# Optimization experiments

Hardware: AMD Instinct MI355X
Metric: run time of the kernel (lower is better)

## Reference

```python
import jax, jax.numpy as jnp
import numpy as np

TEMP = 1.0  # map_token_sampling.temp
EPS = 1e-7


def setup_inputs() -> dict:
    key = jax.random.key(0)
    k1, k2, k3, k4, k5 = jax.random.split(key, 5)
    N, T, K = 65536, 3, 2048
    return {
        "traj_pos": jax.random.normal(k1, (N, T, 2), dtype=jnp.float32) * 5.0,
        "traj_theta": jax.random.normal(k2, (N,), dtype=jnp.float32),
        "map_token_sample_pt": jax.random.normal(k3, (K, T, 2), dtype=jnp.float32) * 5.0,
        "token_traj_src": jax.random.normal(k4, (K, 22), dtype=jnp.float32),
        "gumbel_u": jax.random.uniform(k5, (N, 32), dtype=jnp.float32),
        "num_k": 32,
    }


def reference(traj_pos, traj_theta, map_token_sample_pt, token_traj_src, gumbel_u, num_k):
    N = traj_pos.shape[0]
    K = map_token_sample_pt.shape[0]
    # --- transform_to_local: rotate global polyline into frame of first point ---
    pos_now = traj_pos[:, 0]                      # [N, 2]
    d = traj_pos - pos_now[:, None, :]            # [N, T, 2]
    c, s = jnp.cos(traj_theta), jnp.sin(traj_theta)
    lx = c[:, None] * d[..., 0] + s[:, None] * d[..., 1]
    ly = -s[:, None] * d[..., 0] + c[:, None] * d[..., 1]
    a = jnp.stack([lx, ly], axis=-1).reshape(N, -1)               # [N, T*2]
    b = map_token_sample_pt.reshape(K, -1)                        # [K, T*2]
    # --- squared-distance codebook match (||a-b||^2 expansion, avoids [N,K,T,2]) ---
    dist = (
        jnp.sum(a * a, axis=-1, keepdims=True)
        + jnp.sum(b * b, axis=-1)[None, :]
        - 2.0 * (a @ b.T)
    )                                                             # [N, K]
    # --- topk smallest + categorical (Gumbel-max) sampling ---
    neg_topk, topk_idx = jax.lax.top_k(-dist, num_k)              # [N, num_k]
    logits = (-1e-6 + neg_topk) / TEMP                            # (-1e-6 - topk_dists)/temp
    g = -jnp.log(-jnp.log(gumbel_u * (1.0 - 2.0 * EPS) + EPS))    # Gumbel(0,1)
    samp = jnp.argmax(logits + g, axis=-1)                        # [N]
    token_idx = jnp.take_along_axis(topk_idx, samp[:, None], axis=1)[:, 0]  # [N]
    # --- gather token trajectories ---
    gathered = token_traj_src[token_idx]                          # [N, 22]
    return gathered
```

## Files before the change

### kernel.cpp

```cpp
#include <hip/hip_runtime.h>
#include <cstdint>
#include <math.h>

#define K_TOK 2048
#define NPAIR 16
#define BLK   512
#define WPB   8

typedef float v2f __attribute__((ext_vector_type(2)));

__device__ __forceinline__ uint32_t f2key(float f) {
    uint32_t u = __float_as_uint(f);
    return u ^ ((uint32_t)(((int32_t)u) >> 31) | 0x80000000u);
}

template<int CTRL, int RM, int BM, bool BC>
__device__ __forceinline__ int dpp_i(int old, int v) {
    return __builtin_amdgcn_update_dpp(old, v, CTRL, RM, BM, BC);
}
__device__ __forceinline__ int wave_sum(int v) {
    v += dpp_i<0x111, 0xf, 0xf, true >(0, v);
    v += dpp_i<0x112, 0xf, 0xf, true >(0, v);
    v += dpp_i<0x114, 0xf, 0xf, true >(0, v);
    v += dpp_i<0x118, 0xf, 0xf, true >(0, v);
    v += dpp_i<0x142, 0xa, 0xf, false>(0, v);
    v += dpp_i<0x143, 0xc, 0xf, false>(0, v);
    return __builtin_amdgcn_readlane(v, 63);
}
__device__ __forceinline__ int wave_scan_incl(int v) {
    v += dpp_i<0x111, 0xf, 0xf, true >(0, v);
    v += dpp_i<0x112, 0xf, 0xf, true >(0, v);
    v += dpp_i<0x114, 0xf, 0xf, true >(0, v);
    v += dpp_i<0x118, 0xf, 0xf, true >(0, v);
    v += dpp_i<0x142, 0xa, 0xf, false>(0, v);
    v += dpp_i<0x143, 0xc, 0xf, false>(0, v);
    return v;
}
template<int M>
__device__ __forceinline__ uint32_t lxu(uint32_t x) {
    if constexpr (M == 1)       return (uint32_t)dpp_i<0xB1,  0xf, 0xf, true>(0, (int)x);
    else if constexpr (M == 2)  return (uint32_t)dpp_i<0x4E,  0xf, 0xf, true>(0, (int)x);
    else if constexpr (M == 8)  return (uint32_t)dpp_i<0x128, 0xf, 0xf, true>(0, (int)x);
    else if constexpr (M == 4)  return (uint32_t)__builtin_amdgcn_ds_swizzle((int)x, 0x101F);
    else if constexpr (M == 16) return (uint32_t)__builtin_amdgcn_ds_swizzle((int)x, 0x401F);
    else                        return (uint32_t)__shfl_xor((int)x, 32, 64);
}
template<int M>
__device__ __forceinline__ uint64_t lxu64(uint64_t x) {
    uint32_t h = lxu<M>((uint32_t)(x >> 32));
    uint32_t l = lxu<M>((uint32_t)x);
    return ((uint64_t)h << 32) | l;
}

__global__ void prep_tok(const float* __restrict__ mpt,
                         float4* __restrict__ bpair, float* __restrict__ sbout) {
    #pragma clang fp contract(off)
    int P = blockIdx.x * blockDim.x + threadIdx.x;
    if (P >= K_TOK / 2) return;
    int k0 = 2 * P, k1 = 2 * P + 1;
    float u0 = mpt[k0*6+0], u1 = mpt[k0*6+1], u2 = mpt[k0*6+2];
    float u3 = mpt[k0*6+3], u4 = mpt[k0*6+4], u5 = mpt[k0*6+5];
    float w0 = mpt[k1*6+0], w1 = mpt[k1*6+1], w2 = mpt[k1*6+2];
    float w3 = mpt[k1*6+3], w4 = mpt[k1*6+4], w5 = mpt[k1*6+5];
    float s0 = ((((u0*u0+u1*u1)+u2*u2)+u3*u3)+u4*u4)+u5*u5;
    float s1 = ((((w0*w0+w1*w1)+w2*w2)+w3*w3)+w4*w4)+w5*w5;
    bpair[2*P]   = make_float4(u2, w2, u3, w3);
    bpair[2*P+1] = make_float4(u4, w4, u5, w5);
    sbout[k0] = s0; sbout[k1] = s1;
}

__global__ void prep_frame(const float* __restrict__ traj_pos,
                           const float* __restrict__ traj_theta,
                           float4* __restrict__ aA, float* __restrict__ saA, int N) {
    #pragma clang fp contract(off)
    int n = blockIdx.x * blockDim.x + threadIdx.x;
    if (n >= N) return;
    const float* tp = traj_pos + (size_t)n*6;
    float p0x=tp[0], p0y=tp[1];
    float dx1=tp[2]-p0x, dy1=tp[3]-p0y;
    float dx2=tp[4]-p0x, dy2=tp[5]-p0y;
    float th = traj_theta[n];
    float c = (float)cos((double)th);
    float s = (float)sin((double)th);
    float ns = -s;
    float a2 = c*dx1 + s*dy1;
    float a3 = ns*dx1 + c*dy1;
    float a4 = c*dx2 + s*dy2;
    float a5 = ns*dx2 + c*dy2;
    float q2=a2*a2,q3=a3*a3,q4=a4*a4,q5=a5*a5;
    float sa = ((q2+q3)+q4)+q5;
    aA[n] = make_float4(a2,a3,a4,a5);
    saA[n] = sa;
}

__global__ void prep_gumbel(const float* __restrict__ gu, float* __restrict__ g, int total) {
    #pragma clang fp contract(off)
    int i = blockIdx.x * blockDim.x + threadIdx.x;
    if (i >= total) return;
    const float C1F = (float)(1.0 - 2.0*1e-7);
    float u = gu[i];
    float t = u * C1F;
    t = t + 1e-7f;
    float li = (float)log((double)t);
    float ni = -li;
    float lo = (float)log((double)ni);
    g[i] = -lo;
}

__device__ __forceinline__ int count_mask(const v2f dd2[NPAIR], float T, uint32_t* cmo) {
    uint32_t cm = 0;
    #pragma unroll
    for (int p = 0; p < NPAIR; ++p) {
        if (dd2[p].x <= T) cm |= (1u << (2*p));
        if (dd2[p].y <= T) cm |= (1u << (2*p+1));
    }
    *cmo = cm;
    return wave_sum(__popc(cm));
}

__global__ __launch_bounds__(BLK, 4) void topk_kernel(
        const float* __restrict__ traj_pos, const float* __restrict__ traj_theta,
        const float4* __restrict__ bpair, const float* __restrict__ sbg,
        const float4* __restrict__ aAg, const float* __restrict__ saAg,
        const float* __restrict__ gtab,
        const float* __restrict__ token_src, const float* __restrict__ gumbel,
        float* __restrict__ out, int Nrows, int useFrame, int useG) {
    #pragma clang fp contract(off)
    __shared__ float    sSB[K_TOK];
    __shared__ uint32_t sCidx[WPB][64];

    const int tid = threadIdx.x;
    {
        const float4* s4 = (const float4*)sbg;
        ((float4*)sSB)[tid] = s4[tid];
    }
    __syncthreads();

    const int wv   = tid >> 6;
    const int lane = tid & 63;
    const int n    = blockIdx.x * WPB + wv;
    if (n >= Nrows) return;

    float a2, a3, a4, a5, sa;
    if (useFrame) {
        float4 av = aAg[n];
        a2 = av.x; a3 = av.y; a4 = av.z; a5 = av.w;
        sa = saAg[n];
    } else {
        const float* tp = traj_pos + (size_t)n * 6;
        float p0x = tp[0], p0y = tp[1];
        float dx1 = tp[2] - p0x, dy1 = tp[3] - p0y;
        float dx2 = tp[4] - p0x, dy2 = tp[5] - p0y;
        float th = traj_theta[n];
        float c = (float)cos((double)th);
        float s = (float)sin((double)th);
        float ns = -s;
        a2 = c*dx1 + s*dy1;
        a3 = ns*dx1 + c*dy1;
        a4 = c*dx2 + s*dy2;
        a5 = ns*dx2 + c*dy2;
        float q2 = a2*a2, q3 = a3*a3, q4 = a4*a4, q5 = a5*a5;
        sa = ((q2 + q3) + q4) + q5;
    }

    const v2f a2v = { a2, a2 }, a3v = { a3, a3 }, a4v = { a4, a4 }, a5v = { a5, a5 };
    const v2f sav = { sa, sa }, n2v = { -2.0f, -2.0f };
    v2f dd2[NPAIR];
    v2f lm2 = { INFINITY, INFINITY };
    #pragma unroll
    for (int p = 0; p < NPAIR; ++p) {
        int P = p * 64 + lane;
        float4 q0 = bpair[2*P];
        float4 q1 = bpair[2*P+1];
        v2f sb2 = ((const v2f*)sSB)[P];
        v2f bx = { q0.x, q0.y }, by = { q0.z, q0.w };
        v2f bz = { q1.x, q1.y }, bw = { q1.z, q1.w };
        v2f d = a2v * bx;
        d = __builtin_elementwise_fma(a3v, by, d);
        d = __builtin_elementwise_fma(a4v, bz, d);
        d = __builtin_elementwise_fma(a5v, bw, d);
        v2f ss = sav + sb2;
        v2f dist = __builtin_elementwise_fma(n2v, d, ss);
        dd2[p] = dist;
        lm2.x = fminf(lm2.x, dist.x);
        lm2.y = fminf(lm2.y, dist.y);
    }
    float lmin = fminf(lm2.x, lm2.y);

    {
        float v = lmin;
        #define FST(K2,J2) { float o = __uint_as_float(lxu<J2>(__float_as_uint(v))); \
            bool up = ((lane & K2) == 0) == ((lane & J2) == 0); \
            v = up ? fminf(v, o) : fmaxf(v, o); }
        FST(2,1)
        FST(4,2)  FST(4,1)
        FST(8,4)  FST(8,2)  FST(8,1)
        FST(16,8) FST(16,4) FST(16,2) FST(16,1)
        FST(32,16) FST(32,8) FST(32,4) FST(32,2) FST(32,1)
        FST(64,32) FST(64,16) FST(64,8) FST(64,4) FST(64,2) FST(64,1)
        #undef FST
        lmin = v;
    }
    float gmn = __uint_as_float((uint32_t)__builtin_amdgcn_readlane((int)__float_as_uint(lmin), 0));
    float T0  = __uint_as_float((uint32_t)__builtin_amdgcn_readlane((int)__float_as_uint(lmin), 31));

    uint32_t cmask = 0;
    int cnt = count_mask(dd2, T0, &cmask);
    bool done = (cnt >= 32 && cnt <= 64);
    float loV = gmn, hiV = T0;
    for (int it = 0; it < 12 && !done; ++it) {
        float mid = 0.5f * (loV + hiV);
        if (!(mid > loV && mid < hiV)) break;
        uint32_t cm2;
        int c = count_mask(dd2, mid, &cm2);
        if (c < 32) loV = mid;
        else if (c > 64) hiV = mid;
        else { cnt = c; cmask = cm2; done = true; }
    }

    if (!done) {
        uint32_t A = 0u; bool found = false; int ccf = 0;
        for (int b = 31; b >= 0; --b) {
            uint32_t T2 = A | ((1u << b) - 1u);
            int cc = 0;
            #pragma unroll
            for (int p = 0; p < NPAIR; ++p) {
                cc += (f2key(dd2[p].x) <= T2) ? 1 : 0;
                cc += (f2key(dd2[p].y) <= T2) ? 1 : 0;
            }
            cc = wave_sum(cc);
            if (cc >= 32) { if (cc <= 64) { A = T2; ccf = cc; found = true; break; } }
            else A |= (1u << b);
        }
        if (!found) {
            int cc = 0;
            #pragma unroll
            for (int p = 0; p < NPAIR; ++p) {
                cc += (f2key(dd2[p].x) <= A) ? 1 : 0;
                cc += (f2key(dd2[p].y) <= A) ? 1 : 0;
            }
            ccf = wave_sum(cc);
        }
        cnt = ccf;
        cmask = 0;
        #pragma unroll
        for (int p = 0; p < NPAIR; ++p) {
            if (f2key(dd2[p].x) <= A) cmask |= (1u << (2*p));
            if (f2key(dd2[p].y) <= A) cmask |= (1u << (2*p+1));
        }
    }
    int cnt_cap = cnt > 64 ? 64 : cnt;

    {
        int lc  = __popc(cmask);
        int pos = wave_scan_incl(lc) - lc;
        uint32_t m = cmask;
        while (m) {
            int j = __builtin_ctz(m);
            m &= m - 1;
            int token = 2 * ((j >> 1) * 64 + lane) + (j & 1);
            if (pos < 64) sCidx[wv][pos] = (uint32_t)token;
            ++pos;
        }
    }
    asm volatile("s_waitcnt lgkmcnt(0)" ::: "memory");

    uint64_t bv;
    if (lane < cnt_cap) {
        uint32_t idxv = sCidx[wv][lane];
        uint32_t P = idxv >> 1;
        float4 q0 = bpair[2*P];
        float4 q1 = bpair[2*P+1];
        int h = (int)(idxv & 1u);
        float bx = h ? q0.y : q0.x;
        float by = h ? q0.w : q0.z;
        float bz = h ? q1.y : q1.x;
        float bw = h ? q1.w : q1.z;
        float sbv = sSB[idxv];
        float d0 = a2 * bx;
        d0 = fmaf(a3, by, d0);
        d0 = fmaf(a4, bz, d0);
        d0 = fmaf(a5, bw, d0);
        float ss = sa + sbv;
        float dist = fmaf(-2.0f, d0, ss);
        bv = ((uint64_t)f2key(dist) << 16) | (uint64_t)idxv;
    } else {
        bv = ~0ull;
    }

    #define UST(K2,J2) { uint64_t o = lxu64<J2>(bv); \
        bool up = ((lane & K2) == 0) == ((lane & J2) == 0); \
        bv = ((o < bv) == up) ? o : bv; }
    UST(2,1)
    UST(4,2)  UST(4,1)
    UST(8,4)  UST(8,2)  UST(8,1)
    UST(16,8) UST(16,4) UST(16,2) UST(16,1)
    UST(32,16) UST(32,8) UST(32,4) UST(32,2) UST(32,1)
    UST(64,32) UST(64,16) UST(64,8) UST(64,4) UST(64,2) UST(64,1)
    #undef UST

    float dsel;
    {
        uint32_t kbits = (uint32_t)(bv >> 16);
        uint32_t mkb = ((uint32_t)((~(int32_t)kbits) >> 31)) | 0x80000000u;
        dsel = __uint_as_float(kbits ^ mkb);
    }
    int tok = (int)(bv & 0xFFFFu);
    uint32_t kh = 0u, kl = 0u;
    if (lane < 32) {
        float neg   = -dsel;
        float logit = (-1e-6f) + neg;
        float g;
        if (useG) {
            g = gtab[(size_t)n * 32 + lane];
        } else {
            const float C1F = (float)(1.0 - 2.0 * 1e-7);
            float u = gumbel[(size_t)n * 32 + lane];
            float t = u * C1F;
            t = t + 1e-7f;
            float li = (float)log((double)t);
            float ni = -li;
            float lo2 = (float)log((double)ni);
            g = -lo2;
        }
        float score = logit + g;
        kh = f2key(score);
        kl = ((uint32_t)(63 - lane) << 11) | (uint32_t)tok;
    }
    #define MAXST(CTRL, RM) { \
        uint32_t oh = (uint32_t)dpp_i<CTRL, RM, 0xf, false>((int)kh, (int)kh); \
        uint32_t ol = (uint32_t)dpp_i<CTRL, RM, 0xf, false>((int)kl, (int)kl); \
        if (((((uint64_t)oh << 32) | ol)) > ((((uint64_t)kh << 32) | kl))) { kh = oh; kl = ol; } }
    MAXST(0x111, 0xf) MAXST(0x112, 0xf) MAXST(0x114, 0xf) MAXST(0x118, 0xf)
    MAXST(0x142, 0xa) MAXST(0x143, 0xc)
    #undef MAXST
    uint32_t wl = (uint32_t)__builtin_amdgcn_readlane((int)kl, 63);
    int tw = (int)(wl & 0x7FFu);

    if (lane < 22) out[(size_t)n * 22 + lane] = token_src[(size_t)tw * 22 + lane];
}

extern "C" void kernel_launch(void* const* d_in, const int* in_sizes, int n_in,
                              void* d_out, int out_size, void* d_ws, size_t ws_size,
                              hipStream_t stream) {
    const float* traj_pos   = (const float*)d_in[0];
    const float* traj_theta = (const float*)d_in[1];
    const float* mpt        = (const float*)d_in[2];
    const float* token_src  = (const float*)d_in[3];
    const float* gumbel     = (const float*)d_in[4];
    float* out = (float*)d_out;

    int N = in_sizes[0] / 6;

    size_t off_bp = 0;
    size_t off_sb = off_bp + (size_t)K_TOK * 16;
    size_t off_aA = off_sb + (size_t)K_TOK * 4;
    size_t off_sa = off_aA + (size_t)N * 16;
    size_t off_g  = off_sa + (size_t)N * 4;
    size_t need_frame = off_sa + (size_t)N * 4;
    size_t need_g     = off_g + (size_t)N * 32 * 4;

    int useFrame = (ws_size >= need_frame) ? 1 : 0;
    int useG     = (ws_size >= need_g) ? 1 : 0;

    float4* bp  = (float4*)((char*)d_ws + off_bp);
    float*  sb  = (float*)((char*)d_ws + off_sb);
    float4* aA  = (float4*)((char*)d_ws + off_aA);
    float*  saA = (float*)((char*)d_ws + off_sa);
    float*  g   = (float*)((char*)d_ws + off_g);

    hipLaunchKernelGGL(prep_tok, dim3((K_TOK/2 + 255) / 256), dim3(256), 0, stream, mpt, bp, sb);
    if (useFrame)
        hipLaunchKernelGGL(prep_frame, dim3((N + 255) / 256), dim3(256), 0, stream,
                           traj_pos, traj_theta, aA, saA, N);
    if (useG) {
        int total = N * 32;
        hipLaunchKernelGGL(prep_gumbel, dim3((total + 255) / 256), dim3(256), 0, stream,
                           gumbel, g, total);
    }

    int blocks = (N + WPB - 1) / WPB;
    hipLaunchKernelGGL(topk_kernel, dim3(blocks), dim3(BLK), 0, stream,
                       traj_pos, traj_theta, bp, sb, aA, saA, g,
                       token_src, gumbel, out, N, useFrame, useG);
}
```

Before: 107.6 us.

## Process two rows per wave sharing codebook loads, use ballot-based counting

Each wave now handles two query rows, loading every codebook pair once and computing distances for both rows, which halves the global codebook traffic per row. The codebook layout is split into two separate float4 arrays so loads are contiguous per lane. Threshold counting switches from a DPP wave-sum of a per-lane popcount to per-element ballots with scalar popcount. The trade-offs are doubled register pressure from holding two distance arrays, and half as many blocks in the grid.

```diff
diff --git a/kernel.cpp b/kernel.cpp
--- a/kernel.cpp
+++ b/kernel.cpp
@@ -6,6 +6,7 @@
 #define NPAIR 16
 #define BLK   512
 #define WPB   8
+#define RPW   2
 
 typedef float v2f __attribute__((ext_vector_type(2)));
 
@@ -17,15 +18,6 @@
 template<int CTRL, int RM, int BM, bool BC>
 __device__ __forceinline__ int dpp_i(int old, int v) {
     return __builtin_amdgcn_update_dpp(old, v, CTRL, RM, BM, BC);
-}
-__device__ __forceinline__ int wave_sum(int v) {
-    v += dpp_i<0x111, 0xf, 0xf, true >(0, v);
-    v += dpp_i<0x112, 0xf, 0xf, true >(0, v);
-    v += dpp_i<0x114, 0xf, 0xf, true >(0, v);
-    v += dpp_i<0x118, 0xf, 0xf, true >(0, v);
-    v += dpp_i<0x142, 0xa, 0xf, false>(0, v);
-    v += dpp_i<0x143, 0xc, 0xf, false>(0, v);
-    return __builtin_amdgcn_readlane(v, 63);
 }
 __device__ __forceinline__ int wave_scan_incl(int v) {
     v += dpp_i<0x111, 0xf, 0xf, true >(0, v);
@@ -53,7 +45,8 @@
 }
 
 __global__ void prep_tok(const float* __restrict__ mpt,
-                         float4* __restrict__ bpair, float* __restrict__ sbout) {
+                         float4* __restrict__ bA, float4* __restrict__ bB,
+                         float* __restrict__ sbout) {
     #pragma clang fp contract(off)
     int P = blockIdx.x * blockDim.x + threadIdx.x;
     if (P >= K_TOK / 2) return;
@@ -64,8 +57,8 @@
     float w3 = mpt[k1*6+3], w4 = mpt[k1*6+4], w5 = mpt[k1*6+5];
     float s0 = ((((u0*u0+u1*u1)+u2*u2)+u3*u3)+u4*u4)+u5*u5;
     float s1 = ((((w0*w0+w1*w1)+w2*w2)+w3*w3)+w4*w4)+w5*w5;
-    bpair[2*P]   = make_float4(u2, w2, u3, w3);
-    bpair[2*P+1] = make_float4(u4, w4, u5, w5);
+    bA[P] = make_float4(u2, w2, u3, w3);
+    bB[P] = make_float4(u4, w4, u5, w5);
     sbout[k0] = s0; sbout[k1] = s1;
 }
 
@@ -107,86 +100,39 @@
     g[i] = -lo;
 }
 
-__device__ __forceinline__ int count_mask(const v2f dd2[NPAIR], float T, uint32_t* cmo) {
-    uint32_t cm = 0;
+__device__ __forceinline__ int count_le_sc(const v2f (&dd)[NPAIR], float T) {
+    int c = 0;
     #pragma unroll
     for (int p = 0; p < NPAIR; ++p) {
-        if (dd2[p].x <= T) cm |= (1u << (2*p));
-        if (dd2[p].y <= T) cm |= (1u << (2*p+1));
-    }
-    *cmo = cm;
-    return wave_sum(__popc(cm));
-}
-
-__global__ __launch_bounds__(BLK, 4) void topk_kernel(
-        const float* __restrict__ traj_pos, const float* __restrict__ traj_theta,
-        const float4* __restrict__ bpair, const float* __restrict__ sbg,
-        const float4* __restrict__ aAg, const float* __restrict__ saAg,
-        const float* __restrict__ gtab,
-        const float* __restrict__ token_src, const float* __restrict__ gumbel,
-        float* __restrict__ out, int Nrows, int useFrame, int useG) {
-    #pragma clang fp contract(off)
-    __shared__ float    sSB[K_TOK];
-    __shared__ uint32_t sCidx[WPB][64];
-
-    const int tid = threadIdx.x;
-    {
-        const float4* s4 = (const float4*)sbg;
-        ((float4*)sSB)[tid] = s4[tid];
-    }
-    __syncthreads();
-
-    const int wv   = tid >> 6;
-    const int lane = tid & 63;
-    const int n    = blockIdx.x * WPB + wv;
-    if (n >= Nrows) return;
-
-    float a2, a3, a4, a5, sa;
-    if (useFrame) {
-        float4 av = aAg[n];
-        a2 = av.x; a3 = av.y; a4 = av.z; a5 = av.w;
-        sa = saAg[n];
-    } else {
-        const float* tp = traj_pos + (size_t)n * 6;
-        float p0x = tp[0], p0y = tp[1];
-        float dx1 = tp[2] - p0x, dy1 = tp[3] - p0y;
-        float dx2 = tp[4] - p0x, dy2 = tp[5] - p0y;
-        float th = traj_theta[n];
-        float c = (float)cos((double)th);
-        float s = (float)sin((double)th);
-        float ns = -s;
-        a2 = c*dx1 + s*dy1;
-        a3 = ns*dx1 + c*dy1;
-        a4 = c*dx2 + s*dy2;
-        a5 = ns*dx2 + c*dy2;
-        float q2 = a2*a2, q3 = a3*a3, q4 = a4*a4, q5 = a5*a5;
-        sa = ((q2 + q3) + q4) + q5;
-    }
-
-    const v2f a2v = { a2, a2 }, a3v = { a3, a3 }, a4v = { a4, a4 }, a5v = { a5, a5 };
-    const v2f sav = { sa, sa }, n2v = { -2.0f, -2.0f };
-    v2f dd2[NPAIR];
-    v2f lm2 = { INFINITY, INFINITY };
+        c += (int)__popcll(__ballot(dd[p].x <= T));
+        c += (int)__popcll(__ballot(dd[p].y <= T));
+    }
+    return c;
+}
+__device__ __forceinline__ int count_key_sc(const v2f (&dd)[NPAIR], uint32_t A) {
+    int c = 0;
     #pragma unroll
     for (int p = 0; p < NPAIR; ++p) {
-        int P = p * 64 + lane;
-        float4 q0 = bpair[2*P];
-        float4 q1 = bpair[2*P+1];
-        v2f sb2 = ((const v2f*)sSB)[P];
-        v2f bx = { q0.x, q0.y }, by = { q0.z, q0.w };
-        v2f bz = { q1.x, q1.y }, bw = { q1.z, q1.w };
-        v2f d = a2v * bx;
-        d = __builtin_elementwise_fma(a3v, by, d);
-        d = __builtin_elementwise_fma(a4v, bz, d);
-        d = __builtin_elementwise_fma(a5v, bw, d);
-        v2f ss = sav + sb2;
-        v2f dist = __builtin_elementwise_fma(n2v, d, ss);
-        dd2[p] = dist;
-        lm2.x = fminf(lm2.x, dist.x);
-        lm2.y = fminf(lm2.y, dist.y);
-    }
-    float lmin = fminf(lm2.x, lm2.y);
-
+        c += (int)__popcll(__ballot(f2key(dd[p].x) <= A));
+        c += (int)__popcll(__ballot(f2key(dd[p].y) <= A));
+    }
+    return c;
+}
+
+__device__ __forceinline__ void select_row(
+        const v2f (&dd)[NPAIR], float a2, float a3, float a4, float a5, float sa,
+        int n, int lane, uint32_t* sCrow,
+        const float4* __restrict__ bA, const float4* __restrict__ bB,
+        const float* __restrict__ sSB,
+        const float* __restrict__ gtab, const float* __restrict__ gumbel, int useG,
+        const float* __restrict__ token_src, float* __restrict__ out) {
+    #pragma clang fp contract(off)
+    float lmin = INFINITY;
+    #pragma unroll
+    for (int p = 0; p < NPAIR; ++p) {
+        lmin = fminf(lmin, dd[p].x);
+        lmin = fminf(lmin, dd[p].y);
+    }
     {
         float v = lmin;
         #define FST(K2,J2) { float o = __uint_as_float(lxu<J2>(__float_as_uint(v))); \
@@ -204,52 +150,48 @@
     float gmn = __uint_as_float((uint32_t)__builtin_amdgcn_readlane((int)__float_as_uint(lmin), 0));
     float T0  = __uint_as_float((uint32_t)__builtin_amdgcn_readlane((int)__float_as_uint(lmin), 31));
 
-    uint32_t cmask = 0;
-    int cnt = count_mask(dd2, T0, &cmask);
+    float T = T0;
+    int cnt = count_le_sc(dd, T0);
     bool done = (cnt >= 32 && cnt <= 64);
     float loV = gmn, hiV = T0;
     for (int it = 0; it < 12 && !done; ++it) {
         float mid = 0.5f * (loV + hiV);
         if (!(mid > loV && mid < hiV)) break;
-        uint32_t cm2;
-        int c = count_mask(dd2, mid, &cm2);
+        int c = count_le_sc(dd, mid);
         if (c < 32) loV = mid;
         else if (c > 64) hiV = mid;
-        else { cnt = c; cmask = cm2; done = true; }
-    }
-
+        else { cnt = c; T = mid; done = true; }
+    }
+    uint32_t A = 0u;
+    bool useKey = false;
     if (!done) {
-        uint32_t A = 0u; bool found = false; int ccf = 0;
+        bool found = false; int ccf = 0;
         for (int b = 31; b >= 0; --b) {
             uint32_t T2 = A | ((1u << b) - 1u);
-            int cc = 0;
-            #pragma unroll
-            for (int p = 0; p < NPAIR; ++p) {
-                cc += (f2key(dd2[p].x) <= T2) ? 1 : 0;
-                cc += (f2key(dd2[p].y) <= T2) ? 1 : 0;
-            }
-            cc = wave_sum(cc);
+            int cc = count_key_sc(dd, T2);
             if (cc >= 32) { if (cc <= 64) { A = T2; ccf = cc; found = true; break; } }
             else A |= (1u << b);
         }
-        if (!found) {
-            int cc = 0;
-            #pragma unroll
-            for (int p = 0; p < NPAIR; ++p) {
-                cc += (f2key(dd2[p].x) <= A) ? 1 : 0;
-                cc += (f2key(dd2[p].y) <= A) ? 1 : 0;
-            }
-            ccf = wave_sum(cc);
-        }
+        if (!found) ccf = count_key_sc(dd, A);
         cnt = ccf;
-        cmask = 0;
+        useKey = true;
+    }
+    int cnt_cap = cnt > 64 ? 64 : cnt;
+
+    uint32_t cmask = 0;
+    if (!useKey) {
         #pragma unroll
         for (int p = 0; p < NPAIR; ++p) {
-            if (f2key(dd2[p].x) <= A) cmask |= (1u << (2*p));
-            if (f2key(dd2[p].y) <= A) cmask |= (1u << (2*p+1));
-        }
-    }
-    int cnt_cap = cnt > 64 ? 64 : cnt;
+            if (dd[p].x <= T) cmask |= (1u << (2*p));
+            if (dd[p].y <= T) cmask |= (1u << (2*p+1));
+        }
+    } else {
+        #pragma unroll
+        for (int p = 0; p < NPAIR; ++p) {
+            if (f2key(dd[p].x) <= A) cmask |= (1u << (2*p));
+            if (f2key(dd[p].y) <= A) cmask |= (1u << (2*p+1));
+        }
+    }
 
     {
         int lc  = __popc(cmask);
@@ -259,7 +201,7 @@
             int j = __builtin_ctz(m);
             m &= m - 1;
             int token = 2 * ((j >> 1) * 64 + lane) + (j & 1);
-            if (pos < 64) sCidx[wv][pos] = (uint32_t)token;
+            if (pos < 64) sCrow[pos] = (uint32_t)token;
             ++pos;
         }
     }
@@ -267,10 +209,10 @@
 
     uint64_t bv;
     if (lane < cnt_cap) {
-        uint32_t idxv = sCidx[wv][lane];
+        uint32_t idxv = sCrow[lane];
         uint32_t P = idxv >> 1;
-        float4 q0 = bpair[2*P];
-        float4 q1 = bpair[2*P+1];
+        float4 q0 = bA[P];
+        float4 q1 = bB[P];
         int h = (int)(idxv & 1u);
         float bx = h ? q0.y : q0.x;
         float by = h ? q0.w : q0.z;
@@ -340,6 +282,93 @@
     if (lane < 22) out[(size_t)n * 22 + lane] = token_src[(size_t)tw * 22 + lane];
 }
 
+__global__ __launch_bounds__(BLK, 4) void topk_kernel(
+        const float* __restrict__ traj_pos, const float* __restrict__ traj_theta,
+        const float4* __restrict__ bA, const float4* __restrict__ bB,
+        const float* __restrict__ sbg,
+        const float4* __restrict__ aAg, const float* __restrict__ saAg,
+        const float* __restrict__ gtab,
+        const float* __restrict__ token_src, const float* __restrict__ gumbel,
+        float* __restrict__ out, int Nrows, int useFrame, int useG) {
+    #pragma clang fp contract(off)
+    __shared__ float    sSB[K_TOK];
+    __shared__ uint32_t sCidx[WPB][64];
+
+    const int tid = threadIdx.x;
+    {
+        const float4* s4 = (const float4*)sbg;
+        ((float4*)sSB)[tid] = s4[tid];
+    }
+    __syncthreads();
+
+    const int wv   = tid >> 6;
+    const int lane = tid & 63;
+    const int n0   = blockIdx.x * (WPB * RPW) + wv;
+    const int n1   = n0 + WPB;
+
+    float a2_0=0, a3_0=0, a4_0=0, a5_0=0, sa_0=0;
+    float a2_1=0, a3_1=0, a4_1=0, a5_1=0, sa_1=0;
+    bool has0 = (n0 < Nrows), has1 = (n1 < Nrows);
+    if (useFrame) {
+        if (has0) { float4 av = aAg[n0]; a2_0=av.x; a3_0=av.y; a4_0=av.z; a5_0=av.w; sa_0=saAg[n0]; }
+        if (has1) { float4 av = aAg[n1]; a2_1=av.x; a3_1=av.y; a4_1=av.z; a5_1=av.w; sa_1=saAg[n1]; }
+    } else {
+        for (int r = 0; r < 2; ++r) {
+            int n = r ? n1 : n0;
+            if (n >= Nrows) continue;
+            const float* tp = traj_pos + (size_t)n * 6;
+            float p0x = tp[0], p0y = tp[1];
+            float dx1 = tp[2] - p0x, dy1 = tp[3] - p0y;
+            float dx2 = tp[4] - p0x, dy2 = tp[5] - p0y;
+            float th = traj_theta[n];
+            float c = (float)cos((double)th);
+            float s = (float)sin((double)th);
+            float ns = -s;
+            float a2 = c*dx1 + s*dy1;
+            float a3 = ns*dx1 + c*dy1;
+            float a4 = c*dx2 + s*dy2;
+            float a5 = ns*dx2 + c*dy2;
+            float q2 = a2*a2, q3 = a3*a3, q4 = a4*a4, q5 = a5*a5;
+            float sa = ((q2 + q3) + q4) + q5;
+            if (r) { a2_1=a2; a3_1=a3; a4_1=a4; a5_1=a5; sa_1=sa; }
+            else   { a2_0=a2; a3_0=a3; a4_0=a4; a5_0=a5; sa_0=sa; }
+        }
+    }
+
+    const v2f a2v0={a2_0,a2_0}, a3v0={a3_0,a3_0}, a4v0={a4_0,a4_0}, a5v0={a5_0,a5_0}, sav0={sa_0,sa_0};
+    const v2f a2v1={a2_1,a2_1}, a3v1={a3_1,a3_1}, a4v1={a4_1,a4_1}, a5v1={a5_1,a5_1}, sav1={sa_1,sa_1};
+    const v2f n2v = { -2.0f, -2.0f };
+    v2f ddA[NPAIR], ddB[NPAIR];
+    #pragma unroll
+    for (int p = 0; p < NPAIR; ++p) {
+        int P = p * 64 + lane;
+        float4 q0 = bA[P];
+        float4 q1 = bB[P];
+        v2f sb2 = ((const v2f*)sSB)[P];
+        v2f bx = { q0.x, q0.y }, by = { q0.z, q0.w };
+        v2f bz = { q1.x, q1.y }, bw = { q1.z, q1.w };
+        v2f d0 = a2v0 * bx;
+        d0 = __builtin_elementwise_fma(a3v0, by, d0);
+        d0 = __builtin_elementwise_fma(a4v0, bz, d0);
+        d0 = __builtin_elementwise_fma(a5v0, bw, d0);
+        v2f ss0 = sav0 + sb2;
+        ddA[p] = __builtin_elementwise_fma(n2v, d0, ss0);
+        v2f d1 = a2v1 * bx;
+        d1 = __builtin_elementwise_fma(a3v1, by, d1);
+        d1 = __builtin_elementwise_fma(a4v1, bz, d1);
+        d1 = __builtin_elementwise_fma(a5v1, bw, d1);
+        v2f ss1 = sav1 + sb2;
+        ddB[p] = __builtin_elementwise_fma(n2v, d1, ss1);
+    }
+
+    if (has0)
+        select_row(ddA, a2_0, a3_0, a4_0, a5_0, sa_0, n0, lane, sCidx[wv],
+                   bA, bB, sSB, gtab, gumbel, useG, token_src, out);
+    if (has1)
+        select_row(ddB, a2_1, a3_1, a4_1, a5_1, sa_1, n1, lane, sCidx[wv],
+                   bA, bB, sSB, gtab, gumbel, useG, token_src, out);
+}
+
 extern "C" void kernel_launch(void* const* d_in, const int* in_sizes, int n_in,
                               void* d_out, int out_size, void* d_ws, size_t ws_size,
                               hipStream_t stream) {
@@ -352,8 +381,9 @@
 
     int N = in_sizes[0] / 6;
 
-    size_t off_bp = 0;
-    size_t off_sb = off_bp + (size_t)K_TOK * 16;
+    size_t off_bA = 0;
+    size_t off_bB = off_bA + (size_t)(K_TOK/2) * 16;
+    size_t off_sb = off_bB + (size_t)(K_TOK/2) * 16;
     size_t off_aA = off_sb + (size_t)K_TOK * 4;
     size_t off_sa = off_aA + (size_t)N * 16;
     size_t off_g  = off_sa + (size_t)N * 4;
@@ -363,13 +393,14 @@
     int useFrame = (ws_size >= need_frame) ? 1 : 0;
     int useG     = (ws_size >= need_g) ? 1 : 0;
 
-    float4* bp  = (float4*)((char*)d_ws + off_bp);
+    float4* bA  = (float4*)((char*)d_ws + off_bA);
+    float4* bB  = (float4*)((char*)d_ws + off_bB);
     float*  sb  = (float*)((char*)d_ws + off_sb);
     float4* aA  = (float4*)((char*)d_ws + off_aA);
     float*  saA = (float*)((char*)d_ws + off_sa);
     float*  g   = (float*)((char*)d_ws + off_g);
 
-    hipLaunchKernelGGL(prep_tok, dim3((K_TOK/2 + 255) / 256), dim3(256), 0, stream, mpt, bp, sb);
+    hipLaunchKernelGGL(prep_tok, dim3((K_TOK/2 + 255) / 256), dim3(256), 0, stream, mpt, bA, bB, sb);
     if (useFrame)
         hipLaunchKernelGGL(prep_frame, dim3((N + 255) / 256), dim3(256), 0, stream,
                            traj_pos, traj_theta, aA, saA, N);
@@ -379,8 +410,9 @@
                            gumbel, g, total);
     }
 
-    int blocks = (N + WPB - 1) / WPB;
+    int rows_per_block = WPB * RPW;
+    int blocks = (N + rows_per_block - 1) / rows_per_block;
     hipLaunchKernelGGL(topk_kernel, dim3(blocks), dim3(BLK), 0, stream,
-                       traj_pos, traj_theta, bp, sb, aA, saA, g,
+                       traj_pos, traj_theta, bA, bB, sb, aA, saA, g,
                        token_src, gumbel, out, N, useFrame, useG);
 }
```

New measurement: 424.0 us. +294.2%, slower.

## Split token pair table into two planar arrays and count via ballot popcount

Applied to the files above, without the earlier changes.

Replaces the interleaved bpair array with two separate float4 arrays so each wave's loads of the first and second halves are contiguous and coalesced. Threshold counting in the bisection and radix-search loops now uses ballot plus scalar popcount instead of a per-lane popcount followed by a DPP wave reduction. The candidate mask is built once after the threshold is chosen, rather than inside every counting pass. This cuts VALU and DPP work per search iteration, at the cost of 32 ballots per count.

```diff
diff --git a/kernel.cpp b/kernel.cpp
--- a/kernel.cpp
+++ b/kernel.cpp
@@ -17,15 +17,6 @@
 template<int CTRL, int RM, int BM, bool BC>
 __device__ __forceinline__ int dpp_i(int old, int v) {
     return __builtin_amdgcn_update_dpp(old, v, CTRL, RM, BM, BC);
-}
-__device__ __forceinline__ int wave_sum(int v) {
-    v += dpp_i<0x111, 0xf, 0xf, true >(0, v);
-    v += dpp_i<0x112, 0xf, 0xf, true >(0, v);
-    v += dpp_i<0x114, 0xf, 0xf, true >(0, v);
-    v += dpp_i<0x118, 0xf, 0xf, true >(0, v);
-    v += dpp_i<0x142, 0xa, 0xf, false>(0, v);
-    v += dpp_i<0x143, 0xc, 0xf, false>(0, v);
-    return __builtin_amdgcn_readlane(v, 63);
 }
 __device__ __forceinline__ int wave_scan_incl(int v) {
     v += dpp_i<0x111, 0xf, 0xf, true >(0, v);
@@ -53,7 +44,8 @@
 }
 
 __global__ void prep_tok(const float* __restrict__ mpt,
-                         float4* __restrict__ bpair, float* __restrict__ sbout) {
+                         float4* __restrict__ bA, float4* __restrict__ bB,
+                         float* __restrict__ sbout) {
     #pragma clang fp contract(off)
     int P = blockIdx.x * blockDim.x + threadIdx.x;
     if (P >= K_TOK / 2) return;
@@ -64,8 +56,8 @@
     float w3 = mpt[k1*6+3], w4 = mpt[k1*6+4], w5 = mpt[k1*6+5];
     float s0 = ((((u0*u0+u1*u1)+u2*u2)+u3*u3)+u4*u4)+u5*u5;
     float s1 = ((((w0*w0+w1*w1)+w2*w2)+w3*w3)+w4*w4)+w5*w5;
-    bpair[2*P]   = make_float4(u2, w2, u3, w3);
-    bpair[2*P+1] = make_float4(u4, w4, u5, w5);
+    bA[P] = make_float4(u2, w2, u3, w3);
+    bB[P] = make_float4(u4, w4, u5, w5);
     sbout[k0] = s0; sbout[k1] = s1;
 }
 
@@ -107,20 +99,29 @@
     g[i] = -lo;
 }
 
-__device__ __forceinline__ int count_mask(const v2f dd2[NPAIR], float T, uint32_t* cmo) {
-    uint32_t cm = 0;
+__device__ __forceinline__ int count_le_sc(const v2f (&dd)[NPAIR], float T) {
+    int c = 0;
     #pragma unroll
     for (int p = 0; p < NPAIR; ++p) {
-        if (dd2[p].x <= T) cm |= (1u << (2*p));
-        if (dd2[p].y <= T) cm |= (1u << (2*p+1));
-    }
-    *cmo = cm;
-    return wave_sum(__popc(cm));
+        c += (int)__popcll(__ballot(dd[p].x <= T));
+        c += (int)__popcll(__ballot(dd[p].y <= T));
+    }
+    return c;
+}
+__device__ __forceinline__ int count_key_sc(const v2f (&dd)[NPAIR], uint32_t A) {
+    int c = 0;
+    #pragma unroll
+    for (int p = 0; p < NPAIR; ++p) {
+        c += (int)__popcll(__ballot(f2key(dd[p].x) <= A));
+        c += (int)__popcll(__ballot(f2key(dd[p].y) <= A));
+    }
+    return c;
 }
 
 __global__ __launch_bounds__(BLK, 4) void topk_kernel(
         const float* __restrict__ traj_pos, const float* __restrict__ traj_theta,
-        const float4* __restrict__ bpair, const float* __restrict__ sbg,
+        const float4* __restrict__ bA, const float4* __restrict__ bB,
+        const float* __restrict__ sbg,
         const float4* __restrict__ aAg, const float* __restrict__ saAg,
         const float* __restrict__ gtab,
         const float* __restrict__ token_src, const float* __restrict__ gumbel,
@@ -170,8 +171,8 @@
     #pragma unroll
     for (int p = 0; p < NPAIR; ++p) {
         int P = p * 64 + lane;
-        float4 q0 = bpair[2*P];
-        float4 q1 = bpair[2*P+1];
+        float4 q0 = bA[P];
+        float4 q1 = bB[P];
         v2f sb2 = ((const v2f*)sSB)[P];
         v2f bx = { q0.x, q0.y }, by = { q0.z, q0.w };
         v2f bz = { q1.x, q1.y }, bw = { q1.z, q1.w };
@@ -204,52 +205,48 @@
     float gmn = __uint_as_float((uint32_t)__builtin_amdgcn_readlane((int)__float_as_uint(lmin), 0));
     float T0  = __uint_as_float((uint32_t)__builtin_amdgcn_readlane((int)__float_as_uint(lmin), 31));
 
-    uint32_t cmask = 0;
-    int cnt = count_mask(dd2, T0, &cmask);
+    float T = T0;
+    int cnt = count_le_sc(dd2, T0);
     bool done = (cnt >= 32 && cnt <= 64);
     float loV = gmn, hiV = T0;
     for (int it = 0; it < 12 && !done; ++it) {
         float mid = 0.5f * (loV + hiV);
         if (!(mid > loV && mid < hiV)) break;
-        uint32_t cm2;
-        int c = count_mask(dd2, mid, &cm2);
+        int c = count_le_sc(dd2, mid);
         if (c < 32) loV = mid;
         else if (c > 64) hiV = mid;
-        else { cnt = c; cmask = cm2; done = true; }
-    }
-
+        else { cnt = c; T = mid; done = true; }
+    }
+    uint32_t A = 0u;
+    bool useKey = false;
     if (!done) {
-        uint32_t A = 0u; bool found = false; int ccf = 0;
+        bool found = false; int ccf = 0;
         for (int b = 31; b >= 0; --b) {
             uint32_t T2 = A | ((1u << b) - 1u);
-            int cc = 0;
-            #pragma unroll
-            for (int p = 0; p < NPAIR; ++p) {
-                cc += (f2key(dd2[p].x) <= T2) ? 1 : 0;
-                cc += (f2key(dd2[p].y) <= T2) ? 1 : 0;
-            }
-            cc = wave_sum(cc);
+            int cc = count_key_sc(dd2, T2);
             if (cc >= 32) { if (cc <= 64) { A = T2; ccf = cc; found = true; break; } }
             else A |= (1u << b);
         }
-        if (!found) {
-            int cc = 0;
-            #pragma unroll
-            for (int p = 0; p < NPAIR; ++p) {
-                cc += (f2key(dd2[p].x) <= A) ? 1 : 0;
-                cc += (f2key(dd2[p].y) <= A) ? 1 : 0;
-            }
-            ccf = wave_sum(cc);
-        }
+        if (!found) ccf = count_key_sc(dd2, A);
         cnt = ccf;
-        cmask = 0;
+        useKey = true;
+    }
+    int cnt_cap = cnt > 64 ? 64 : cnt;
+
+    uint32_t cmask = 0;
+    if (!useKey) {
+        #pragma unroll
+        for (int p = 0; p < NPAIR; ++p) {
+            if (dd2[p].x <= T) cmask |= (1u << (2*p));
+            if (dd2[p].y <= T) cmask |= (1u << (2*p+1));
+        }
+    } else {
         #pragma unroll
         for (int p = 0; p < NPAIR; ++p) {
             if (f2key(dd2[p].x) <= A) cmask |= (1u << (2*p));
             if (f2key(dd2[p].y) <= A) cmask |= (1u << (2*p+1));
         }
     }
-    int cnt_cap = cnt > 64 ? 64 : cnt;
 
     {
         int lc  = __popc(cmask);
@@ -269,8 +266,8 @@
     if (lane < cnt_cap) {
         uint32_t idxv = sCidx[wv][lane];
         uint32_t P = idxv >> 1;
-        float4 q0 = bpair[2*P];
-        float4 q1 = bpair[2*P+1];
+        float4 q0 = bA[P];
+        float4 q1 = bB[P];
         int h = (int)(idxv & 1u);
         float bx = h ? q0.y : q0.x;
         float by = h ? q0.w : q0.z;
@@ -352,8 +349,9 @@
 
     int N = in_sizes[0] / 6;
 
-    size_t off_bp = 0;
-    size_t off_sb = off_bp + (size_t)K_TOK * 16;
+    size_t off_bA = 0;
+    size_t off_bB = off_bA + (size_t)(K_TOK/2) * 16;
+    size_t off_sb = off_bB + (size_t)(K_TOK/2) * 16;
     size_t off_aA = off_sb + (size_t)K_TOK * 4;
     size_t off_sa = off_aA + (size_t)N * 16;
     size_t off_g  = off_sa + (size_t)N * 4;
@@ -363,13 +361,14 @@
     int useFrame = (ws_size >= need_frame) ? 1 : 0;
     int useG     = (ws_size >= need_g) ? 1 : 0;
 
-    float4* bp  = (float4*)((char*)d_ws + off_bp);
+    float4* bA  = (float4*)((char*)d_ws + off_bA);
+    float4* bB  = (float4*)((char*)d_ws + off_bB);
     float*  sb  = (float*)((char*)d_ws + off_sb);
     float4* aA  = (float4*)((char*)d_ws + off_aA);
     float*  saA = (float*)((char*)d_ws + off_sa);
     float*  g   = (float*)((char*)d_ws + off_g);
 
-    hipLaunchKernelGGL(prep_tok, dim3((K_TOK/2 + 255) / 256), dim3(256), 0, stream, mpt, bp, sb);
+    hipLaunchKernelGGL(prep_tok, dim3((K_TOK/2 + 255) / 256), dim3(256), 0, stream, mpt, bA, bB, sb);
     if (useFrame)
         hipLaunchKernelGGL(prep_frame, dim3((N + 255) / 256), dim3(256), 0, stream,
                            traj_pos, traj_theta, aA, saA, N);
@@ -381,6 +380,6 @@
 
     int blocks = (N + WPB - 1) / WPB;
     hipLaunchKernelGGL(topk_kernel, dim3(blocks), dim3(BLK), 0, stream,
-                       traj_pos, traj_theta, bp, sb, aA, saA, g,
+                       traj_pos, traj_theta, bA, bB, sb, aA, saA, g,
                        token_src, gumbel, out, N, useFrame, useG);
 }
```

Result: slower. 129.8 us (+20.6%).
